# Kernel tuning notes

Hardware: AMD Instinct MI355X
Metric: run time of the kernel (lower is better)

Reference implementation:

```python
import jax, jax.numpy as jnp
import numpy as np

N = 8192        # nodes
F_IN = 512      # input feature dim
H1 = 256        # args.hidden1
H2 = 64         # args.hidden2
E = 262144      # edges (avg degree 32)


def setup_inputs() -> dict:
    key = jax.random.key(0)
    ks = jax.random.split(key, 7)
    x = jax.random.normal(ks[0], (N, F_IN), dtype=jnp.float32)
    adj_rows = jax.random.randint(ks[1], (E,), 0, N, dtype=jnp.int32)
    adj_cols = jax.random.randint(ks[2], (E,), 0, N, dtype=jnp.int32)
    adj_vals = jax.random.uniform(ks[3], (E,), dtype=jnp.float32)
    # Xavier-uniform init like reset_parameters()
    def xavier(k, fan_in, fan_out):
        lim = jnp.sqrt(6.0 / (fan_in + fan_out))
        return jax.random.uniform(k, (fan_in, fan_out), jnp.float32, -lim, lim)
    W1 = xavier(ks[4], F_IN, H1)
    W2 = xavier(ks[5], H1, H2)
    W3 = xavier(ks[6], H1, H2)
    return {"x": x, "adj_rows": adj_rows, "adj_cols": adj_cols,
            "adj_vals": adj_vals, "W1": W1, "W2": W2, "W3": W3}


def reference(x, adj_rows, adj_cols, adj_vals, W1, W2, W3):
    n = x.shape[0]

    def spmm(support):
        # sparse [N,N] @ dense [N,D]: gather neighbor rows, scale, scatter-add
        return jax.ops.segment_sum(adj_vals[:, None] * support[adj_cols],
                                   adj_rows, num_segments=n)

    # gc1: dropout(no-op, eval) -> x @ W1 -> SpMM -> relu
    h1 = jax.nn.relu(spmm(x @ W1))
    # gc2 / gc3: identity activation
    mu = spmm(h1 @ W2)
    logvar = spmm(h1 @ W3)
    z = mu  # eval-mode reparameterize returns mu
    # InnerProductDecoder with identity act (dropout no-op in eval)
    adj_recon = z @ z.T  # [N, N]
    return adj_recon, z, mu, logvar
```

## Files before the change

### kernel.cpp

```cpp
#include <hip/hip_runtime.h>
#include <hip/hip_bf16.h>

#define N_NODES 8192
#define F_INDIM 512
#define H1DIM   256
#define H2DIM   64

typedef __bf16 bf16x8 __attribute__((ext_vector_type(8)));
typedef __bf16 bf16x4 __attribute__((ext_vector_type(4)));
typedef __bf16 bf16x2 __attribute__((ext_vector_type(2)));
typedef float  floatx4 __attribute__((ext_vector_type(4)));

__global__ void count_rows(const int* __restrict__ rows, int* __restrict__ cnt, int e) {
    int i = blockIdx.x * blockDim.x + threadIdx.x;
    if (i < e) atomicAdd(&cnt[rows[i]], 1);
}

__global__ void scan_rows(const int* __restrict__ cnt, int* __restrict__ row_ptr,
                          int* __restrict__ cursor, int n) {
    __shared__ int sums[1024];
    int t = threadIdx.x;
    int base = t * 8;
    int loc[8];
    int s = 0;
#pragma unroll
    for (int i = 0; i < 8; ++i) { loc[i] = cnt[base + i]; s += loc[i]; }
    sums[t] = s;
    __syncthreads();
    for (int off = 1; off < 1024; off <<= 1) {
        int v = (t >= off) ? sums[t - off] : 0;
        __syncthreads();
        sums[t] += v;
        __syncthreads();
    }
    int run = sums[t] - s;
#pragma unroll
    for (int i = 0; i < 8; ++i) {
        row_ptr[base + i] = run;
        cursor[base + i]  = run;
        run += loc[i];
    }
    if (t == 1023) row_ptr[n] = run;
}

__global__ void scatter_edges(const int* __restrict__ rows, const int* __restrict__ cols,
                              const float* __restrict__ vals, int* __restrict__ cursor,
                              int* __restrict__ csr_col, float* __restrict__ csr_val, int e) {
    int i = blockIdx.x * blockDim.x + threadIdx.x;
    if (i < e) {
        int r = rows[i];
        int slot = atomicAdd(&cursor[r], 1);
        csr_col[slot] = cols[i];
        csr_val[slot] = vals[i];
    }
}

__global__ __launch_bounds__(256) void cast_split_x(const float* __restrict__ x,
                                                    __bf16* __restrict__ xh,
                                                    __bf16* __restrict__ xl) {
    int i = (blockIdx.x * 256 + threadIdx.x) * 4;
    floatx4 v = *(const floatx4*)&x[i];
    bf16x4 h, l;
#pragma unroll
    for (int j = 0; j < 4; ++j) {
        __bf16 hv = (__bf16)v[j];
        h[j] = hv;
        l[j] = (__bf16)(v[j] - (float)hv);
    }
    *(bf16x4*)&xh[i] = h;
    *(bf16x4*)&xl[i] = l;
}

__global__ void transpose_cast_w(const float* __restrict__ W1, const float* __restrict__ W2,
                                 const float* __restrict__ W3,
                                 __bf16* __restrict__ w1th, __bf16* __restrict__ w1tl,
                                 __bf16* __restrict__ w23th, __bf16* __restrict__ w23tl) {
    const int z = blockIdx.z;
    const float* src; __bf16 *oh, *ol; int K, N, rowoff, outld;
    if (z == 0)      { src = W1; K = 512; N = 256; oh = w1th;  ol = w1tl;  rowoff = 0;  outld = 512; }
    else if (z == 1) { src = W2; K = 256; N = 64;  oh = w23th; ol = w23tl; rowoff = 0;  outld = 256; }
    else             { src = W3; K = 256; N = 64;  oh = w23th; ol = w23tl; rowoff = 64; outld = 256; }
    const int kt = blockIdx.x, nt = blockIdx.y;
    if (kt * 32 >= K || nt * 32 >= N) return;
    __shared__ float tile[32][33];
    const int tx = threadIdx.x, ty = threadIdx.y;
#pragma unroll
    for (int j = 0; j < 4; ++j)
        tile[ty + 8 * j][tx] = src[(size_t)(kt * 32 + ty + 8 * j) * N + nt * 32 + tx];
    __syncthreads();
#pragma unroll
    for (int j = 0; j < 4; ++j) {
        int n = nt * 32 + ty + 8 * j;
        int k = kt * 32 + tx;
        float v = tile[tx][ty + 8 * j];
        __bf16 h = (__bf16)v;
        oh[(size_t)(rowoff + n) * outld + k] = h;
        ol[(size_t)(rowoff + n) * outld + k] = (__bf16)(v - (float)h);
    }
}

__global__ __launch_bounds__(256) void gemm1_mfma(const __bf16* __restrict__ xh,
                                                  const __bf16* __restrict__ xl,
                                                  const __bf16* __restrict__ bth,
                                                  const __bf16* __restrict__ btl,
                                                  float* __restrict__ C) {
    constexpr int K = F_INDIM, NN = H1DIM, LDSW = 40;
    __shared__ __bf16 Ah[64 * LDSW], Al[64 * LDSW], Bh[64 * LDSW], Bl[64 * LDSW];
    const int tid = threadIdx.x;
    const int m0 = blockIdx.y * 64, n0 = blockIdx.x * 64;
    const int lane = tid & 63, wv = tid >> 6;
    const int wm = wv >> 1, wn = wv & 1;
    const int r16 = lane & 15, q = lane >> 4;
    const int sr = tid >> 2, sc = (tid & 3) * 8;
    floatx4 acc[2][2] = {};

    for (int k0 = 0; k0 < K; k0 += 32) {
        bf16x8 va  = *(const bf16x8*)&xh [(size_t)(m0 + sr) * K + k0 + sc];
        bf16x8 vb  = *(const bf16x8*)&bth[(size_t)(n0 + sr) * K + k0 + sc];
        bf16x8 va2 = *(const bf16x8*)&xl [(size_t)(m0 + sr) * K + k0 + sc];
        bf16x8 vb2 = *(const bf16x8*)&btl[(size_t)(n0 + sr) * K + k0 + sc];
        __syncthreads();
        *(bf16x8*)&Ah[sr * LDSW + sc] = va;
        *(bf16x8*)&Bh[sr * LDSW + sc] = vb;
        *(bf16x8*)&Al[sr * LDSW + sc] = va2;
        *(bf16x8*)&Bl[sr * LDSW + sc] = vb2;
        __syncthreads();
        bf16x8 ah[2], al[2], bh[2], bl[2];
#pragma unroll
        for (int mt = 0; mt < 2; ++mt) {
            ah[mt] = *(const bf16x8*)&Ah[(wm * 32 + mt * 16 + r16) * LDSW + q * 8];
            al[mt] = *(const bf16x8*)&Al[(wm * 32 + mt * 16 + r16) * LDSW + q * 8];
        }
#pragma unroll
        for (int nt = 0; nt < 2; ++nt) {
            bh[nt] = *(const bf16x8*)&Bh[(wn * 32 + nt * 16 + r16) * LDSW + q * 8];
            bl[nt] = *(const bf16x8*)&Bl[(wn * 32 + nt * 16 + r16) * LDSW + q * 8];
        }
#pragma unroll
        for (int mt = 0; mt < 2; ++mt)
#pragma unroll
            for (int nt = 0; nt < 2; ++nt) {
                acc[mt][nt] = __builtin_amdgcn_mfma_f32_16x16x32_bf16(ah[mt], bh[nt], acc[mt][nt], 0, 0, 0);
                acc[mt][nt] = __builtin_amdgcn_mfma_f32_16x16x32_bf16(ah[mt], bl[nt], acc[mt][nt], 0, 0, 0);
                acc[mt][nt] = __builtin_amdgcn_mfma_f32_16x16x32_bf16(al[mt], bh[nt], acc[mt][nt], 0, 0, 0);
            }
    }
#pragma unroll
    for (int mt = 0; mt < 2; ++mt)
#pragma unroll
        for (int nt = 0; nt < 2; ++nt)
#pragma unroll
            for (int i = 0; i < 4; ++i) {
                int row = m0 + wm * 32 + mt * 16 + q * 4 + i;
                int col = n0 + wn * 32 + nt * 16 + r16;
                C[(size_t)row * NN + col] = acc[mt][nt][i];
            }
}

__global__ __launch_bounds__(256) void spmm_h1(const int* __restrict__ row_ptr,
                                               const int* __restrict__ csr_col,
                                               const float* __restrict__ csr_val,
                                               const float* __restrict__ in,
                                               __bf16* __restrict__ h1h,
                                               __bf16* __restrict__ h1l) {
    __shared__ int   s_col[2][128];
    __shared__ float s_val[2][128];
    __shared__ int   s_deg[2];
    const int tid = threadIdx.x;
    const int half = tid >> 7;
    const int d = tid & 127;
    const int r = blockIdx.x * 2 + half;
    const int beg = row_ptr[r];
    const int deg = row_ptr[r + 1] - beg;
    if (d == 0) s_deg[half] = deg;
    __syncthreads();
    const int trips = (max(s_deg[0], s_deg[1]) + 127) >> 7;
    const float2* in2 = (const float2*)in;
    float ax = 0.f, ay = 0.f;
    for (int t = 0; t < trips; ++t) {
        int base = t * 128;
        __syncthreads();
        if (base + d < deg) {
            s_col[half][d] = csr_col[beg + base + d];
            s_val[half][d] = csr_val[beg + base + d];
        }
        __syncthreads();
        int m = deg - base; if (m > 128) m = 128; if (m < 0) m = 0;
        int e = 0;
        for (; e + 4 <= m; e += 4) {
            float2 x0 = in2[(size_t)s_col[half][e]     * 128 + d];
            float2 x1 = in2[(size_t)s_col[half][e + 1] * 128 + d];
            float2 x2 = in2[(size_t)s_col[half][e + 2] * 128 + d];
            float2 x3 = in2[(size_t)s_col[half][e + 3] * 128 + d];
            float v0 = s_val[half][e], v1 = s_val[half][e + 1];
            float v2 = s_val[half][e + 2], v3 = s_val[half][e + 3];
            ax += v0 * x0.x + v1 * x1.x + v2 * x2.x + v3 * x3.x;
            ay += v0 * x0.y + v1 * x1.y + v2 * x2.y + v3 * x3.y;
        }
        for (; e < m; ++e) {
            float2 xv = in2[(size_t)s_col[half][e] * 128 + d];
            float v = s_val[half][e];
            ax += v * xv.x;
            ay += v * xv.y;
        }
    }
    float rx = fmaxf(ax, 0.f), ry = fmaxf(ay, 0.f);
    __bf16 hx = (__bf16)rx, hy = (__bf16)ry;
    bf16x2 hv = {hx, hy};
    bf16x2 lv = {(__bf16)(rx - (float)hx), (__bf16)(ry - (float)hy)};
    *(bf16x2*)&h1h[(size_t)r * H1DIM + d * 2] = hv;
    *(bf16x2*)&h1l[(size_t)r * H1DIM + d * 2] = lv;
}

__global__ __launch_bounds__(256) void gemm23_mfma(const __bf16* __restrict__ ag_h,
                                                   const __bf16* __restrict__ ag_l,
                                                   const __bf16* __restrict__ bth,
                                                   const __bf16* __restrict__ btl,
                                                   float* __restrict__ t2,
                                                   float* __restrict__ t3) {
    constexpr int K = H1DIM, LDSW = 40;
    __shared__ __bf16 Ah[32 * LDSW], Al[32 * LDSW], Bh[128 * LDSW], Bl[128 * LDSW];
    const int tid = threadIdx.x;
    const int m0 = blockIdx.x * 32;
    const int lane = tid & 63, wn = tid >> 6;
    const int r16 = lane & 15, q = lane >> 4;
    const int ta = tid & 127;
    const int ar = ta >> 2, ac = (ta & 3) * 8;
    floatx4 acc[2][2] = {};

    for (int k0 = 0; k0 < K; k0 += 32) {
        const __bf16* asrc = (tid < 128) ? ag_h : ag_l;
        bf16x8 va = *(const bf16x8*)&asrc[(size_t)(m0 + ar) * K + k0 + ac];
        bf16x8 vbh[2], vbl[2];
#pragma unroll
        for (int v = 0; v < 2; ++v) {
            int id = tid + v * 256;
            int br = id >> 2, bc = (id & 3) * 8;
            vbh[v] = *(const bf16x8*)&bth[(size_t)br * K + k0 + bc];
            vbl[v] = *(const bf16x8*)&btl[(size_t)br * K + k0 + bc];
        }
        __syncthreads();
        {
            __bf16* adst = (tid < 128) ? Ah : Al;
            *(bf16x8*)&adst[ar * LDSW + ac] = va;
        }
#pragma unroll
        for (int v = 0; v < 2; ++v) {
            int id = tid + v * 256;
            int br = id >> 2, bc = (id & 3) * 8;
            *(bf16x8*)&Bh[br * LDSW + bc] = vbh[v];
            *(bf16x8*)&Bl[br * LDSW + bc] = vbl[v];
        }
        __syncthreads();
        bf16x8 ah[2], al[2], bh[2], bl[2];
#pragma unroll
        for (int mt = 0; mt < 2; ++mt) {
            ah[mt] = *(const bf16x8*)&Ah[(mt * 16 + r16) * LDSW + q * 8];
            al[mt] = *(const bf16x8*)&Al[(mt * 16 + r16) * LDSW + q * 8];
        }
#pragma unroll
        for (int nt = 0; nt < 2; ++nt) {
            bh[nt] = *(const bf16x8*)&Bh[(wn * 32 + nt * 16 + r16) * LDSW + q * 8];
            bl[nt] = *(const bf16x8*)&Bl[(wn * 32 + nt * 16 + r16) * LDSW + q * 8];
        }
#pragma unroll
        for (int mt = 0; mt < 2; ++mt)
#pragma unroll
            for (int nt = 0; nt < 2; ++nt) {
                acc[mt][nt] = __builtin_amdgcn_mfma_f32_16x16x32_bf16(ah[mt], bh[nt], acc[mt][nt], 0, 0, 0);
                acc[mt][nt] = __builtin_amdgcn_mfma_f32_16x16x32_bf16(ah[mt], bl[nt], acc[mt][nt], 0, 0, 0);
                acc[mt][nt] = __builtin_amdgcn_mfma_f32_16x16x32_bf16(al[mt], bh[nt], acc[mt][nt], 0, 0, 0);
            }
    }
#pragma unroll
    for (int mt = 0; mt < 2; ++mt)
#pragma unroll
        for (int nt = 0; nt < 2; ++nt)
#pragma unroll
            for (int i = 0; i < 4; ++i) {
                int row = m0 + mt * 16 + q * 4 + i;
                int col = wn * 32 + nt * 16 + r16;
                float vv = acc[mt][nt][i];
                if (col < 64) t2[(size_t)row * H2DIM + col] = vv;
                else          t3[(size_t)row * H2DIM + col - 64] = vv;
            }
}

__global__ __launch_bounds__(256) void spmm_mu_logvar(const int* __restrict__ row_ptr,
                                                      const int* __restrict__ csr_col,
                                                      const float* __restrict__ csr_val,
                                                      const float* __restrict__ t2,
                                                      const float* __restrict__ t3,
                                                      float* __restrict__ mu,
                                                      float* __restrict__ z,
                                                      float* __restrict__ logvar,
                                                      __bf16* __restrict__ zb) {
    __shared__ int   s_col[4][64];
    __shared__ float s_val[4][64];
    __shared__ int   s_deg[4];
    const int tid = threadIdx.x;
    const int rl = tid >> 6;
    const int d = tid & 63;
    const int r = blockIdx.x * 4 + rl;
    const int beg = row_ptr[r];
    const int deg = row_ptr[r + 1] - beg;
    if (d == 0) s_deg[rl] = deg;
    __syncthreads();
    const int md = max(max(s_deg[0], s_deg[1]), max(s_deg[2], s_deg[3]));
    const int trips = (md + 63) >> 6;
    const float2* src2 = (const float2*)((d < 32) ? t2 : t3);
    const int dd = d & 31;
    float ax = 0.f, ay = 0.f;
    for (int t = 0; t < trips; ++t) {
        int base = t * 64;
        __syncthreads();
        if (base + d < deg) {
            s_col[rl][d] = csr_col[beg + base + d];
            s_val[rl][d] = csr_val[beg + base + d];
        }
        __syncthreads();
        int m = deg - base; if (m > 64) m = 64; if (m < 0) m = 0;
        int e = 0;
        for (; e + 4 <= m; e += 4) {
            float2 x0 = src2[(size_t)s_col[rl][e]     * 32 + dd];
            float2 x1 = src2[(size_t)s_col[rl][e + 1] * 32 + dd];
            float2 x2 = src2[(size_t)s_col[rl][e + 2] * 32 + dd];
            float2 x3 = src2[(size_t)s_col[rl][e + 3] * 32 + dd];
            float v0 = s_val[rl][e], v1 = s_val[rl][e + 1];
            float v2 = s_val[rl][e + 2], v3 = s_val[rl][e + 3];
            ax += v0 * x0.x + v1 * x1.x + v2 * x2.x + v3 * x3.x;
            ay += v0 * x0.y + v1 * x1.y + v2 * x2.y + v3 * x3.y;
        }
        for (; e < m; ++e) {
            float2 xv = src2[(size_t)s_col[rl][e] * 32 + dd];
            float v = s_val[rl][e];
            ax += v * xv.x;
            ay += v * xv.y;
        }
    }
    if (d < 32) {
        size_t o2 = (size_t)r * 32 + dd;
        float2 v = {ax, ay};
        ((float2*)mu)[o2] = v;
        ((float2*)z)[o2] = v;
        bf16x2 b = {(__bf16)ax, (__bf16)ay};
        *(bf16x2*)&zb[o2 * 2] = b;
    } else {
        size_t o2 = (size_t)r * 32 + dd;
        float2 v = {ax, ay};
        ((float2*)logvar)[o2] = v;
    }
}

__global__ __launch_bounds__(256) void zzt_mfma(const __bf16* __restrict__ z,
                                                float* __restrict__ C) {
    const int tid = threadIdx.x;
    const int lane = tid & 63;
    const int wave = tid >> 6;
    const int wm = wave >> 1, wn = wave & 1;
    const int m0 = blockIdx.y * 128 + wm * 64;
    const int n0 = blockIdx.x * 128 + wn * 64;
    const int r16 = lane & 15;
    const int quad = lane >> 4;

    floatx4 acc[4][4] = {};
    const char* zb = (const char*)z;

#pragma unroll
    for (int h = 0; h < 2; ++h) {
        bf16x8 a[4], b[4];
#pragma unroll
        for (int mt = 0; mt < 4; ++mt)
            a[mt] = *(const bf16x8*)(zb + (m0 + mt * 16 + r16) * 128 + h * 64 + quad * 16);
#pragma unroll
        for (int nt = 0; nt < 4; ++nt)
            b[nt] = *(const bf16x8*)(zb + (n0 + nt * 16 + r16) * 128 + h * 64 + quad * 16);
#pragma unroll
        for (int mt = 0; mt < 4; ++mt)
#pragma unroll
            for (int nt = 0; nt < 4; ++nt)
                acc[mt][nt] = __builtin_amdgcn_mfma_f32_16x16x32_bf16(a[mt], b[nt], acc[mt][nt], 0, 0, 0);
    }

#pragma unroll
    for (int mt = 0; mt < 4; ++mt)
#pragma unroll
        for (int nt = 0; nt < 4; ++nt)
#pragma unroll
            for (int r = 0; r < 4; ++r) {
                int row = m0 + mt * 16 + quad * 4 + r;
                int col = n0 + nt * 16 + r16;
                C[(size_t)row * N_NODES + col] = acc[mt][nt][r];
            }
}

extern "C" void kernel_launch(void* const* d_in, const int* in_sizes, int n_in,
                              void* d_out, int out_size, void* d_ws, size_t ws_size,
                              hipStream_t stream) {
    const float* x        = (const float*)d_in[0];
    const int*   adj_rows = (const int*)d_in[1];
    const int*   adj_cols = (const int*)d_in[2];
    const float* adj_vals = (const float*)d_in[3];
    const float* W1       = (const float*)d_in[4];
    const float* W2       = (const float*)d_in[5];
    const float* W3       = (const float*)d_in[6];
    const int E = in_sizes[1];
    const int n = N_NODES;

    char* ws = (char*)d_ws;
    size_t off = 0;
    auto alloc = [&](size_t bytes) {
        void* p = ws + off;
        off = (off + bytes + 255) & ~(size_t)255;
        return p;
    };
    int*    cnt     = (int*)alloc((size_t)n * 4);
    int*    row_ptr = (int*)alloc((size_t)(n + 1) * 4);
    int*    cursor  = (int*)alloc((size_t)n * 4);
    int*    csr_col = (int*)alloc((size_t)E * 4);
    float*  csr_val = (float*)alloc((size_t)E * 4);
    __bf16* xh      = (__bf16*)alloc((size_t)n * F_INDIM * 2);
    __bf16* xl      = (__bf16*)alloc((size_t)n * F_INDIM * 2);
    __bf16* w1th    = (__bf16*)alloc((size_t)H1DIM * F_INDIM * 2);
    __bf16* w1tl    = (__bf16*)alloc((size_t)H1DIM * F_INDIM * 2);
    __bf16* w23th   = (__bf16*)alloc((size_t)(2 * H2DIM) * H1DIM * 2);
    __bf16* w23tl   = (__bf16*)alloc((size_t)(2 * H2DIM) * H1DIM * 2);
    float*  support = (float*)alloc((size_t)n * H1DIM * 4);
    __bf16* h1h     = (__bf16*)alloc((size_t)n * H1DIM * 2);
    __bf16* h1l     = (__bf16*)alloc((size_t)n * H1DIM * 2);
    float*  t2      = (float*)alloc((size_t)n * H2DIM * 4);
    float*  t3      = (float*)alloc((size_t)n * H2DIM * 4);
    __bf16* zb      = (__bf16*)alloc((size_t)n * H2DIM * 2);

    float* out        = (float*)d_out;
    float* adj_recon  = out;
    float* z_out      = out + (size_t)n * n;
    float* mu_out     = z_out + (size_t)n * H2DIM;
    float* logvar_out = mu_out + (size_t)n * H2DIM;

    hipMemsetAsync(cnt, 0, (size_t)n * 4, stream);
    count_rows<<<(E + 255) / 256, 256, 0, stream>>>(adj_rows, cnt, E);
    scan_rows<<<1, 1024, 0, stream>>>(cnt, row_ptr, cursor, n);
    scatter_edges<<<(E + 255) / 256, 256, 0, stream>>>(adj_rows, adj_cols, adj_vals,
                                                       cursor, csr_col, csr_val, E);

    cast_split_x<<<(n * F_INDIM) / (256 * 4), 256, 0, stream>>>(x, xh, xl);
    transpose_cast_w<<<dim3(16, 8, 3), dim3(32, 8), 0, stream>>>(W1, W2, W3,
                                                                 w1th, w1tl, w23th, w23tl);

    gemm1_mfma<<<dim3(H1DIM / 64, n / 64), 256, 0, stream>>>(xh, xl, w1th, w1tl, support);
    spmm_h1<<<n / 2, 256, 0, stream>>>(row_ptr, csr_col, csr_val, support, h1h, h1l);

    gemm23_mfma<<<n / 32, 256, 0, stream>>>(h1h, h1l, w23th, w23tl, t2, t3);
    spmm_mu_logvar<<<n / 4, 256, 0, stream>>>(row_ptr, csr_col, csr_val, t2, t3,
                                              mu_out, z_out, logvar_out, zb);

    zzt_mfma<<<dim3(n / 128, n / 128), 256, 0, stream>>>(zb, adj_recon);
}
```

Before: 405.0 us.

## Fuse x cast into GEMM1, wave-per-row SpMM, interleave t2/t3, stage ZZT stores

The cast/split of x to bf16 hi/lo moves into the gemm1 loader, so the separate pass and its intermediate buffers go away. Both SpMM kernels now give one wave per row with no block-wide barriers, and spmm_h1 uses float4 gathers. gemm23 writes t2 and t3 interleaved into one 128-wide buffer. The ZZT kernel stages its output tile in shared memory so global stores are row-contiguous float4 writes, at the cost of extra LDS use and lower occupancy. Shared-memory writes in the SpMM loop are read within the same wave without a barrier, which relies on wave-synchronous execution.

```diff
diff --git a/kernel.cpp b/kernel.cpp
--- a/kernel.cpp
+++ b/kernel.cpp
@@ -53,22 +53,6 @@
         csr_col[slot] = cols[i];
         csr_val[slot] = vals[i];
     }
-}
-
-__global__ __launch_bounds__(256) void cast_split_x(const float* __restrict__ x,
-                                                    __bf16* __restrict__ xh,
-                                                    __bf16* __restrict__ xl) {
-    int i = (blockIdx.x * 256 + threadIdx.x) * 4;
-    floatx4 v = *(const floatx4*)&x[i];
-    bf16x4 h, l;
-#pragma unroll
-    for (int j = 0; j < 4; ++j) {
-        __bf16 hv = (__bf16)v[j];
-        h[j] = hv;
-        l[j] = (__bf16)(v[j] - (float)hv);
-    }
-    *(bf16x4*)&xh[i] = h;
-    *(bf16x4*)&xl[i] = l;
 }
 
 __global__ void transpose_cast_w(const float* __restrict__ W1, const float* __restrict__ W2,
@@ -99,8 +83,7 @@
     }
 }
 
-__global__ __launch_bounds__(256) void gemm1_mfma(const __bf16* __restrict__ xh,
-                                                  const __bf16* __restrict__ xl,
+__global__ __launch_bounds__(256) void gemm1_mfma(const float* __restrict__ x,
                                                   const __bf16* __restrict__ bth,
                                                   const __bf16* __restrict__ btl,
                                                   float* __restrict__ C) {
@@ -115,10 +98,18 @@
     floatx4 acc[2][2] = {};
 
     for (int k0 = 0; k0 < K; k0 += 32) {
-        bf16x8 va  = *(const bf16x8*)&xh [(size_t)(m0 + sr) * K + k0 + sc];
+        floatx4 xa0 = *(const floatx4*)&x[(size_t)(m0 + sr) * K + k0 + sc];
+        floatx4 xa1 = *(const floatx4*)&x[(size_t)(m0 + sr) * K + k0 + sc + 4];
         bf16x8 vb  = *(const bf16x8*)&bth[(size_t)(n0 + sr) * K + k0 + sc];
-        bf16x8 va2 = *(const bf16x8*)&xl [(size_t)(m0 + sr) * K + k0 + sc];
         bf16x8 vb2 = *(const bf16x8*)&btl[(size_t)(n0 + sr) * K + k0 + sc];
+        bf16x8 va, va2;
+#pragma unroll
+        for (int j = 0; j < 4; ++j) {
+            __bf16 h0 = (__bf16)xa0[j];
+            va[j] = h0; va2[j] = (__bf16)(xa0[j] - (float)h0);
+            __bf16 h1 = (__bf16)xa1[j];
+            va[4 + j] = h1; va2[4 + j] = (__bf16)(xa1[j] - (float)h1);
+        }
         __syncthreads();
         *(bf16x8*)&Ah[sr * LDSW + sc] = va;
         *(bf16x8*)&Bh[sr * LDSW + sc] = vb;
@@ -163,61 +154,53 @@
                                                const float* __restrict__ in,
                                                __bf16* __restrict__ h1h,
                                                __bf16* __restrict__ h1l) {
-    __shared__ int   s_col[2][128];
-    __shared__ float s_val[2][128];
-    __shared__ int   s_deg[2];
+    __shared__ int   s_col[4][64];
+    __shared__ float s_val[4][64];
     const int tid = threadIdx.x;
-    const int half = tid >> 7;
-    const int d = tid & 127;
-    const int r = blockIdx.x * 2 + half;
+    const int w = tid >> 6, lane = tid & 63;
+    const int r = blockIdx.x * 4 + w;
     const int beg = row_ptr[r];
     const int deg = row_ptr[r + 1] - beg;
-    if (d == 0) s_deg[half] = deg;
-    __syncthreads();
-    const int trips = (max(s_deg[0], s_deg[1]) + 127) >> 7;
-    const float2* in2 = (const float2*)in;
-    float ax = 0.f, ay = 0.f;
-    for (int t = 0; t < trips; ++t) {
-        int base = t * 128;
-        __syncthreads();
-        if (base + d < deg) {
-            s_col[half][d] = csr_col[beg + base + d];
-            s_val[half][d] = csr_val[beg + base + d];
-        }
-        __syncthreads();
-        int m = deg - base; if (m > 128) m = 128; if (m < 0) m = 0;
+    const floatx4* in4 = (const floatx4*)in;
+    floatx4 acc = {0.f, 0.f, 0.f, 0.f};
+    for (int base = 0; base < deg; base += 64) {
+        int m = deg - base; if (m > 64) m = 64;
+        if (lane < m) {
+            s_col[w][lane] = csr_col[beg + base + lane];
+            s_val[w][lane] = csr_val[beg + base + lane];
+        }
         int e = 0;
         for (; e + 4 <= m; e += 4) {
-            float2 x0 = in2[(size_t)s_col[half][e]     * 128 + d];
-            float2 x1 = in2[(size_t)s_col[half][e + 1] * 128 + d];
-            float2 x2 = in2[(size_t)s_col[half][e + 2] * 128 + d];
-            float2 x3 = in2[(size_t)s_col[half][e + 3] * 128 + d];
-            float v0 = s_val[half][e], v1 = s_val[half][e + 1];
-            float v2 = s_val[half][e + 2], v3 = s_val[half][e + 3];
-            ax += v0 * x0.x + v1 * x1.x + v2 * x2.x + v3 * x3.x;
-            ay += v0 * x0.y + v1 * x1.y + v2 * x2.y + v3 * x3.y;
-        }
-        for (; e < m; ++e) {
-            float2 xv = in2[(size_t)s_col[half][e] * 128 + d];
-            float v = s_val[half][e];
-            ax += v * xv.x;
-            ay += v * xv.y;
-        }
-    }
-    float rx = fmaxf(ax, 0.f), ry = fmaxf(ay, 0.f);
-    __bf16 hx = (__bf16)rx, hy = (__bf16)ry;
-    bf16x2 hv = {hx, hy};
-    bf16x2 lv = {(__bf16)(rx - (float)hx), (__bf16)(ry - (float)hy)};
-    *(bf16x2*)&h1h[(size_t)r * H1DIM + d * 2] = hv;
-    *(bf16x2*)&h1l[(size_t)r * H1DIM + d * 2] = lv;
+            int c0 = s_col[w][e],     c1 = s_col[w][e + 1];
+            int c2 = s_col[w][e + 2], c3 = s_col[w][e + 3];
+            float v0 = s_val[w][e],     v1 = s_val[w][e + 1];
+            float v2 = s_val[w][e + 2], v3 = s_val[w][e + 3];
+            floatx4 x0 = in4[(size_t)c0 * 64 + lane];
+            floatx4 x1 = in4[(size_t)c1 * 64 + lane];
+            floatx4 x2 = in4[(size_t)c2 * 64 + lane];
+            floatx4 x3 = in4[(size_t)c3 * 64 + lane];
+            acc += v0 * x0; acc += v1 * x1; acc += v2 * x2; acc += v3 * x3;
+        }
+        for (; e < m; ++e)
+            acc += s_val[w][e] * in4[(size_t)s_col[w][e] * 64 + lane];
+    }
+    bf16x4 h, l;
+#pragma unroll
+    for (int j = 0; j < 4; ++j) {
+        float rv = fmaxf(acc[j], 0.f);
+        __bf16 hv = (__bf16)rv;
+        h[j] = hv;
+        l[j] = (__bf16)(rv - (float)hv);
+    }
+    *(bf16x4*)&h1h[(size_t)r * H1DIM + lane * 4] = h;
+    *(bf16x4*)&h1l[(size_t)r * H1DIM + lane * 4] = l;
 }
 
 __global__ __launch_bounds__(256) void gemm23_mfma(const __bf16* __restrict__ ag_h,
                                                    const __bf16* __restrict__ ag_l,
                                                    const __bf16* __restrict__ bth,
                                                    const __bf16* __restrict__ btl,
-                                                   float* __restrict__ t2,
-                                                   float* __restrict__ t3) {
+                                                   float* __restrict__ t23) {
     constexpr int K = H1DIM, LDSW = 40;
     __shared__ __bf16 Ah[32 * LDSW], Al[32 * LDSW], Bh[128 * LDSW], Bl[128 * LDSW];
     const int tid = threadIdx.x;
@@ -280,73 +263,62 @@
             for (int i = 0; i < 4; ++i) {
                 int row = m0 + mt * 16 + q * 4 + i;
                 int col = wn * 32 + nt * 16 + r16;
-                float vv = acc[mt][nt][i];
-                if (col < 64) t2[(size_t)row * H2DIM + col] = vv;
-                else          t3[(size_t)row * H2DIM + col - 64] = vv;
+                t23[(size_t)row * 128 + col] = acc[mt][nt][i];
             }
 }
 
 __global__ __launch_bounds__(256) void spmm_mu_logvar(const int* __restrict__ row_ptr,
                                                       const int* __restrict__ csr_col,
                                                       const float* __restrict__ csr_val,
-                                                      const float* __restrict__ t2,
-                                                      const float* __restrict__ t3,
+                                                      const float* __restrict__ t23,
                                                       float* __restrict__ mu,
                                                       float* __restrict__ z,
                                                       float* __restrict__ logvar,
                                                       __bf16* __restrict__ zb) {
     __shared__ int   s_col[4][64];
     __shared__ float s_val[4][64];
-    __shared__ int   s_deg[4];
     const int tid = threadIdx.x;
-    const int rl = tid >> 6;
-    const int d = tid & 63;
-    const int r = blockIdx.x * 4 + rl;
+    const int w = tid >> 6, lane = tid & 63;
+    const int r = blockIdx.x * 4 + w;
     const int beg = row_ptr[r];
     const int deg = row_ptr[r + 1] - beg;
-    if (d == 0) s_deg[rl] = deg;
-    __syncthreads();
-    const int md = max(max(s_deg[0], s_deg[1]), max(s_deg[2], s_deg[3]));
-    const int trips = (md + 63) >> 6;
-    const float2* src2 = (const float2*)((d < 32) ? t2 : t3);
-    const int dd = d & 31;
+    const float2* in2 = (const float2*)t23;
     float ax = 0.f, ay = 0.f;
-    for (int t = 0; t < trips; ++t) {
-        int base = t * 64;
-        __syncthreads();
-        if (base + d < deg) {
-            s_col[rl][d] = csr_col[beg + base + d];
-            s_val[rl][d] = csr_val[beg + base + d];
-        }
-        __syncthreads();
-        int m = deg - base; if (m > 64) m = 64; if (m < 0) m = 0;
+    for (int base = 0; base < deg; base += 64) {
+        int m = deg - base; if (m > 64) m = 64;
+        if (lane < m) {
+            s_col[w][lane] = csr_col[beg + base + lane];
+            s_val[w][lane] = csr_val[beg + base + lane];
+        }
         int e = 0;
         for (; e + 4 <= m; e += 4) {
-            float2 x0 = src2[(size_t)s_col[rl][e]     * 32 + dd];
-            float2 x1 = src2[(size_t)s_col[rl][e + 1] * 32 + dd];
-            float2 x2 = src2[(size_t)s_col[rl][e + 2] * 32 + dd];
-            float2 x3 = src2[(size_t)s_col[rl][e + 3] * 32 + dd];
-            float v0 = s_val[rl][e], v1 = s_val[rl][e + 1];
-            float v2 = s_val[rl][e + 2], v3 = s_val[rl][e + 3];
+            int c0 = s_col[w][e],     c1 = s_col[w][e + 1];
+            int c2 = s_col[w][e + 2], c3 = s_col[w][e + 3];
+            float v0 = s_val[w][e],     v1 = s_val[w][e + 1];
+            float v2 = s_val[w][e + 2], v3 = s_val[w][e + 3];
+            float2 x0 = in2[(size_t)c0 * 64 + lane];
+            float2 x1 = in2[(size_t)c1 * 64 + lane];
+            float2 x2 = in2[(size_t)c2 * 64 + lane];
+            float2 x3 = in2[(size_t)c3 * 64 + lane];
             ax += v0 * x0.x + v1 * x1.x + v2 * x2.x + v3 * x3.x;
             ay += v0 * x0.y + v1 * x1.y + v2 * x2.y + v3 * x3.y;
         }
         for (; e < m; ++e) {
-            float2 xv = src2[(size_t)s_col[rl][e] * 32 + dd];
-            float v = s_val[rl][e];
+            float2 xv = in2[(size_t)s_col[w][e] * 64 + lane];
+            float v = s_val[w][e];
             ax += v * xv.x;
             ay += v * xv.y;
         }
     }
-    if (d < 32) {
-        size_t o2 = (size_t)r * 32 + dd;
+    if (lane < 32) {
+        size_t o2 = (size_t)r * 32 + lane;
         float2 v = {ax, ay};
         ((float2*)mu)[o2] = v;
         ((float2*)z)[o2] = v;
         bf16x2 b = {(__bf16)ax, (__bf16)ay};
-        *(bf16x2*)&zb[o2 * 2] = b;
+        *(bf16x2*)&zb[(size_t)r * H2DIM + lane * 2] = b;
     } else {
-        size_t o2 = (size_t)r * 32 + dd;
+        size_t o2 = (size_t)r * 32 + (lane - 32);
         float2 v = {ax, ay};
         ((float2*)logvar)[o2] = v;
     }
@@ -354,27 +326,30 @@
 
 __global__ __launch_bounds__(256) void zzt_mfma(const __bf16* __restrict__ z,
                                                 float* __restrict__ C) {
+    constexpr int LDT = 132;
+    __shared__ float tile[128 * LDT];
     const int tid = threadIdx.x;
     const int lane = tid & 63;
     const int wave = tid >> 6;
     const int wm = wave >> 1, wn = wave & 1;
-    const int m0 = blockIdx.y * 128 + wm * 64;
-    const int n0 = blockIdx.x * 128 + wn * 64;
+    const int bm = blockIdx.y * 128, bn = blockIdx.x * 128;
+    const int m0 = bm + wm * 64;
+    const int n0 = bn + wn * 64;
     const int r16 = lane & 15;
     const int quad = lane >> 4;
 
     floatx4 acc[4][4] = {};
-    const char* zb = (const char*)z;
+    const char* zc = (const char*)z;
 
 #pragma unroll
     for (int h = 0; h < 2; ++h) {
         bf16x8 a[4], b[4];
 #pragma unroll
         for (int mt = 0; mt < 4; ++mt)
-            a[mt] = *(const bf16x8*)(zb + (m0 + mt * 16 + r16) * 128 + h * 64 + quad * 16);
+            a[mt] = *(const bf16x8*)(zc + (m0 + mt * 16 + r16) * 128 + h * 64 + quad * 16);
 #pragma unroll
         for (int nt = 0; nt < 4; ++nt)
-            b[nt] = *(const bf16x8*)(zb + (n0 + nt * 16 + r16) * 128 + h * 64 + quad * 16);
+            b[nt] = *(const bf16x8*)(zc + (n0 + nt * 16 + r16) * 128 + h * 64 + quad * 16);
 #pragma unroll
         for (int mt = 0; mt < 4; ++mt)
 #pragma unroll
@@ -387,11 +362,16 @@
 #pragma unroll
         for (int nt = 0; nt < 4; ++nt)
 #pragma unroll
-            for (int r = 0; r < 4; ++r) {
-                int row = m0 + mt * 16 + quad * 4 + r;
-                int col = n0 + nt * 16 + r16;
-                C[(size_t)row * N_NODES + col] = acc[mt][nt][r];
-            }
+            for (int rr = 0; rr < 4; ++rr)
+                tile[(wm * 64 + mt * 16 + quad * 4 + rr) * LDT + wn * 64 + nt * 16 + r16] =
+                    acc[mt][nt][rr];
+    __syncthreads();
+
+    for (int i = tid; i < 128 * 32; i += 256) {
+        int rr = i >> 5, cc = (i & 31) * 4;
+        floatx4 v = *(const floatx4*)&tile[rr * LDT + cc];
+        *(floatx4*)&C[(size_t)(bm + rr) * N_NODES + bn + cc] = v;
+    }
 }
 
 extern "C" void kernel_launch(void* const* d_in, const int* in_sizes, int n_in,
@@ -419,8 +399,6 @@
     int*    cursor  = (int*)alloc((size_t)n * 4);
     int*    csr_col = (int*)alloc((size_t)E * 4);
     float*  csr_val = (float*)alloc((size_t)E * 4);
-    __bf16* xh      = (__bf16*)alloc((size_t)n * F_INDIM * 2);
-    __bf16* xl      = (__bf16*)alloc((size_t)n * F_INDIM * 2);
     __bf16* w1th    = (__bf16*)alloc((size_t)H1DIM * F_INDIM * 2);
     __bf16* w1tl    = (__bf16*)alloc((size_t)H1DIM * F_INDIM * 2);
     __bf16* w23th   = (__bf16*)alloc((size_t)(2 * H2DIM) * H1DIM * 2);
@@ -428,8 +406,7 @@
     float*  support = (float*)alloc((size_t)n * H1DIM * 4);
     __bf16* h1h     = (__bf16*)alloc((size_t)n * H1DIM * 2);
     __bf16* h1l     = (__bf16*)alloc((size_t)n * H1DIM * 2);
-    float*  t2      = (float*)alloc((size_t)n * H2DIM * 4);
-    float*  t3      = (float*)alloc((size_t)n * H2DIM * 4);
+    float*  t23     = (float*)alloc((size_t)n * 2 * H2DIM * 4);
     __bf16* zb      = (__bf16*)alloc((size_t)n * H2DIM * 2);
 
     float* out        = (float*)d_out;
@@ -444,15 +421,14 @@
     scatter_edges<<<(E + 255) / 256, 256, 0, stream>>>(adj_rows, adj_cols, adj_vals,
                                                        cursor, csr_col, csr_val, E);
 
-    cast_split_x<<<(n * F_INDIM) / (256 * 4), 256, 0, stream>>>(x, xh, xl);
     transpose_cast_w<<<dim3(16, 8, 3), dim3(32, 8), 0, stream>>>(W1, W2, W3,
                                                                  w1th, w1tl, w23th, w23tl);
 
-    gemm1_mfma<<<dim3(H1DIM / 64, n / 64), 256, 0, stream>>>(xh, xl, w1th, w1tl, support);
-    spmm_h1<<<n / 2, 256, 0, stream>>>(row_ptr, csr_col, csr_val, support, h1h, h1l);
-
-    gemm23_mfma<<<n / 32, 256, 0, stream>>>(h1h, h1l, w23th, w23tl, t2, t3);
-    spmm_mu_logvar<<<n / 4, 256, 0, stream>>>(row_ptr, csr_col, csr_val, t2, t3,
+    gemm1_mfma<<<dim3(H1DIM / 64, n / 64), 256, 0, stream>>>(x, w1th, w1tl, support);
+    spmm_h1<<<n / 4, 256, 0, stream>>>(row_ptr, csr_col, csr_val, support, h1h, h1l);
+
+    gemm23_mfma<<<n / 32, 256, 0, stream>>>(h1h, h1l, w23th, w23tl, t23);
+    spmm_mu_logvar<<<n / 4, 256, 0, stream>>>(row_ptr, csr_col, csr_val, t23,
                                               mu_out, z_out, logvar_out, zb);
 
     zzt_mfma<<<dim3(n / 128, n / 128), 256, 0, stream>>>(zb, adj_recon);
```

Result: no change. 405.2 us (+0.1%).
